# Kernel tuning notes

Hardware: AMD Instinct MI355X
Metric: run time of the kernel (lower is better)

## Reference

```python
import jax, jax.numpy as jnp
import numpy as np

D_MODEL = 1024
D_INTERNAL = 256


def setup_inputs() -> dict:
    key = jax.random.key(0)
    ks = jax.random.split(key, 12)
    s = 0.02
    return {
        "x": jax.random.normal(ks[0], (4, 2048, D_MODEL), dtype=jnp.float32),
        "Wq": jax.random.normal(ks[1], (D_MODEL, D_INTERNAL), dtype=jnp.float32) * s,
        "bq": jnp.zeros((D_INTERNAL,), dtype=jnp.float32),
        "Wk": jax.random.normal(ks[2], (D_MODEL, D_INTERNAL), dtype=jnp.float32) * s,
        "bk": jnp.zeros((D_INTERNAL,), dtype=jnp.float32),
        "Wv": jax.random.normal(ks[3], (D_MODEL, D_MODEL), dtype=jnp.float32) * s,
        "bv": jnp.zeros((D_MODEL,), dtype=jnp.float32),
        "W1": jax.random.normal(ks[4], (D_MODEL, D_MODEL), dtype=jnp.float32) * s,
        "b1": jnp.zeros((D_MODEL,), dtype=jnp.float32),
        "W2": jax.random.normal(ks[5], (D_MODEL, D_MODEL), dtype=jnp.float32) * s,
        "b2": jnp.zeros((D_MODEL,), dtype=jnp.float32),
    }


def reference(x, Wq, bq, Wk, bk, Wv, bv, W1, b1, W2, b2):
    # x: [B, S, D]
    S = x.shape[-2]
    q = x @ Wq + bq            # [B, S, Di]
    k = x @ Wk + bk            # [B, S, Di]
    v = x @ Wv + bv            # [B, S, D]
    scale = 1.0 / jnp.sqrt(jnp.asarray(q.shape[-1], dtype=x.dtype))
    scores = jnp.einsum('bqd,bkd->bqk', q, k) * scale  # [B, S, S]
    causal_mask = jnp.triu(jnp.ones((S, S), dtype=bool), k=1)
    scores = jnp.where(causal_mask, -jnp.inf, scores)
    attn = jax.nn.softmax(scores, axis=-1)             # [B, S, S]
    attention = jnp.einsum('bqk,bkd->bqd', attn, v)    # [B, S, D]
    h = x + attention
    ff = jax.nn.relu(h @ W1 + b1) @ W2 + b2
    return h + ff, attn
```

## Files before the change

kernel.cpp:

```cpp
#include <hip/hip_runtime.h>
#include <hip/hip_bf16.h>

#define BM 128
#define BN 128

typedef __bf16 bf16x8 __attribute__((ext_vector_type(8)));
typedef float f32x4 __attribute__((ext_vector_type(4)));
typedef unsigned short u16;

__device__ __forceinline__ u16 f2bf(float f) {
    __bf16 b = (__bf16)f;
    return __builtin_bit_cast(u16, b);
}
__device__ __forceinline__ float bf2f(u16 u) {
    __bf16 b = __builtin_bit_cast(__bf16, u);
    return (float)b;
}

__device__ __forceinline__ void gload_lds16(const void* g, void* l) {
    __builtin_amdgcn_global_load_lds(
        (const __attribute__((address_space(1))) void*)g,
        (__attribute__((address_space(3))) void*)l,
        16, 0, 0);
}

__device__ __forceinline__ bf16x8 lds_read_b128(const u16* p) {
    bf16x8 r;
    const __attribute__((address_space(3))) u16* lp =
        (const __attribute__((address_space(3))) u16*)p;
    asm volatile("ds_read_b128 %0, %1" : "=v"(r) : "v"(lp));
    return r;
}

template <int MODE>
__global__ __launch_bounds__(256)
void gemm_bt(const u16* __restrict__ A, int lda, long long a_bs,
             const u16* __restrict__ Bt, int ldb, long long b_bs,
             int Kdim, int ldc, long long c_bs,
             const float* __restrict__ bias, float scale,
             const void* __restrict__ resid, long long r_bs,
             void* __restrict__ out, int causal)
{
    int bx = blockIdx.x, by = blockIdx.y, bz = blockIdx.z;
    if (causal == 3) {
        const int t = blockIdx.x;
        int byy = (int)((sqrtf(8.f * (float)t + 1.f) - 1.f) * 0.5f);
        while ((byy + 1) * (byy + 2) / 2 <= t) byy++;
        while (byy * (byy + 1) / 2 > t) byy--;
        by = byy; bx = t - byy * (byy + 1) / 2; bz = blockIdx.y;
    }
    if (causal == 2 && bz >= 2) by = (int)gridDim.y - 1 - by;
    const int kend = (causal == 2) ? min(Kdim, (by + 1) * BM) : Kdim;

    A  += (long long)bz * a_bs;
    Bt += (long long)bz * b_bs;

    const int m0 = by * BM, n0 = bx * BN;
    const int tid = threadIdx.x;
    const int wave = tid >> 6, lane = tid & 63;
    const int wy = wave >> 1, wx = wave & 1;
    const int lr = lane >> 2, lc8 = (lane & 3) * 8;
    const int lane15 = lane & 15, kq = lane >> 4;

    __shared__ __align__(16) u16 As[2][BM * 32];
    __shared__ __align__(16) u16 Bs[2][BN * 32];

    f32x4 acc[4][4] = {};

    for (int k0 = 0; k0 < kend; k0 += 64) {
        __syncthreads();
        #pragma unroll
        for (int h = 0; h < 2; h++) {
            const int kh = k0 + h * 32 + lc8;
            #pragma unroll
            for (int it = 0; it < 2; it++) {
                const int row = wave * 16 + it * 64 + lr;
                gload_lds16(A  + (size_t)(m0 + row) * lda + kh,
                            &As[h][(wave * 16 + it * 64) * 32]);
                gload_lds16(Bt + (size_t)(n0 + row) * ldb + kh,
                            &Bs[h][(wave * 16 + it * 64) * 32]);
            }
        }
        __syncthreads();

        #pragma unroll
        for (int h = 0; h < 2; h++) {
            bf16x8 av[4], bv[4];
            #pragma unroll
            for (int i = 0; i < 4; i++)
                av[i] = *(const bf16x8*)&As[h][(wy * 64 + i * 16 + lane15) * 32 + kq * 8];
            #pragma unroll
            for (int j = 0; j < 4; j++)
                bv[j] = *(const bf16x8*)&Bs[h][(wx * 64 + j * 16 + lane15) * 32 + kq * 8];
            #pragma unroll
            for (int i = 0; i < 4; i++)
                #pragma unroll
                for (int j = 0; j < 4; j++)
                    acc[i][j] = __builtin_amdgcn_mfma_f32_16x16x32_bf16(av[i], bv[j], acc[i][j], 0, 0, 0);
        }
    }

    #pragma unroll
    for (int i = 0; i < 4; i++) {
        const int rl = m0 + wy * 64 + i * 16 + kq * 4;
        #pragma unroll
        for (int j = 0; j < 4; j++) {
            const int c = n0 + wx * 64 + j * 16 + lane15;
            #pragma unroll
            for (int rg = 0; rg < 4; rg++) {
                const int r = rl + rg;
                const size_t idx = (size_t)bz * c_bs + (size_t)r * ldc + c;
                const float v = acc[i][j][rg];
                if (MODE == 2) {
                    float p = __expf(v * scale);
                    if (c > r) p = 0.f;
                    ((u16*)out)[idx] = f2bf(p);
                } else if (MODE == 3) {
                    const u16* xr = (const u16*)resid;
                    const float linv = bias[(size_t)bz * 2048 + r];
                    const float h = bf2f(xr[(size_t)bz * r_bs + (size_t)r * ldc + c]) + v * linv;
                    ((u16*)out)[idx] = f2bf(h);
                }
            }
        }
    }
}

template <int MODE>
__global__ __launch_bounds__(512, 2)
void gemm_bt2(const u16* __restrict__ A, int lda,
              const u16* __restrict__ Bt, int ldb,
              int ldc,
              const float* __restrict__ bias,
              const void* __restrict__ resid,
              void* __restrict__ out)
{
    constexpr int NT = 16;
    const int gx = gridDim.x;
    const int nwg = gx * (int)gridDim.y;
    int lin = blockIdx.y * gx + blockIdx.x;
    lin = (lin & 7) * (nwg >> 3) + (lin >> 3);
    const int m0 = (lin / gx) * 256, n0 = (lin % gx) * 128;

    const int tid = threadIdx.x;
    const int wave = tid >> 6, lane = tid & 63;
    const int wr = wave >> 1, wc = wave & 1;
    const int lane15 = lane & 15, kq = lane >> 4;
    const int lr = lane >> 2;
    const int swzc8 = ((lane & 3) ^ ((lane >> 3) & 3)) * 8;
    const int lslot = lane15 * 32 + ((kq ^ ((lane15 >> 1) & 3)) * 8);

    __shared__ __align__(16) u16 As0[2][256 * 32];
    __shared__ __align__(16) u16 As1[2][256 * 32];
    __shared__ __align__(16) u16 As2[2][256 * 32];
    __shared__ __align__(16) u16 Bs0[2][128 * 32];
    __shared__ __align__(16) u16 Bs1[2][128 * 32];
    __shared__ __align__(16) u16 Bs2[2][128 * 32];

    f32x4 acc[4][4] = {};

    auto stage = [&](u16 (*Ad)[256 * 32], u16 (*Bd)[128 * 32], int tt) {
        #pragma unroll
        for (int h = 0; h < 2; h++) {
            const int kh = (tt << 6) + h * 32 + swzc8;
            #pragma unroll
            for (int it = 0; it < 2; it++) {
                const int row = wave * 16 + it * 128 + lr;
                gload_lds16(A + (size_t)(m0 + row) * lda + kh,
                            &Ad[h][(wave * 16 + it * 128) * 32]);
            }
            gload_lds16(Bt + (size_t)(n0 + wave * 16 + lr) * ldb + kh,
                        &Bd[h][(wave * 16) * 32]);
        }
    };

    stage(As0, Bs0, 0);
    stage(As1, Bs1, 1);

    #pragma unroll
    for (int t = 0; t < NT; t++) {
        u16 (*pAc)[256 * 32] = (t % 3 == 0) ? As0 : (t % 3 == 1) ? As1 : As2;
        u16 (*pBc)[128 * 32] = (t % 3 == 0) ? Bs0 : (t % 3 == 1) ? Bs1 : Bs2;
        if (t < NT - 1) asm volatile("s_waitcnt vmcnt(6)" ::: "memory");
        else            asm volatile("s_waitcnt vmcnt(0)" ::: "memory");
        __builtin_amdgcn_s_barrier();
        if (t + 2 < NT) {
            const int tn = (t + 2) % 3;
            u16 (*pAn)[256 * 32] = (tn == 0) ? As0 : (tn == 1) ? As1 : As2;
            u16 (*pBn)[128 * 32] = (tn == 0) ? Bs0 : (tn == 1) ? Bs1 : Bs2;
            stage(pAn, pBn, t + 2);
        }

        bf16x8 av0[4], bv0[4], av1[4], bv1[4];
        #pragma unroll
        for (int i = 0; i < 4; i++)
            av0[i] = lds_read_b128(&pAc[0][(wr * 4 + i) * 512 + lslot]);
        #pragma unroll
        for (int j = 0; j < 4; j++)
            bv0[j] = lds_read_b128(&pBc[0][(wc * 4 + j) * 512 + lslot]);
        #pragma unroll
        for (int i = 0; i < 4; i++)
            av1[i] = lds_read_b128(&pAc[1][(wr * 4 + i) * 512 + lslot]);
        #pragma unroll
        for (int j = 0; j < 4; j++)
            bv1[j] = lds_read_b128(&pBc[1][(wc * 4 + j) * 512 + lslot]);

        asm volatile("s_waitcnt lgkmcnt(8)" ::: "memory");
        __builtin_amdgcn_sched_barrier(0);
        __builtin_amdgcn_s_setprio(1);
        #pragma unroll
        for (int i = 0; i < 4; i++)
            #pragma unroll
            for (int j = 0; j < 4; j++)
                acc[i][j] = __builtin_amdgcn_mfma_f32_16x16x32_bf16(av0[i], bv0[j], acc[i][j], 0, 0, 0);
        __builtin_amdgcn_s_setprio(0);

        asm volatile("s_waitcnt lgkmcnt(0)" ::: "memory");
        __builtin_amdgcn_sched_barrier(0);
        __builtin_amdgcn_s_setprio(1);
        #pragma unroll
        for (int i = 0; i < 4; i++)
            #pragma unroll
            for (int j = 0; j < 4; j++)
                acc[i][j] = __builtin_amdgcn_mfma_f32_16x16x32_bf16(av1[i], bv1[j], acc[i][j], 0, 0, 0);
        __builtin_amdgcn_s_setprio(0);
    }

    if (MODE == 6 && n0 >= 512) {
        u16* o = (u16*)resid;
        #pragma unroll
        for (int i = 0; i < 4; i++) {
            const int r = m0 + wr * 64 + i * 16 + kq * 4;
            const size_t base = (size_t)(r >> 11) * 1024 * 2048 + (r & 2047);
            #pragma unroll
            for (int j = 0; j < 4; j++) {
                const int c = n0 + wc * 64 + j * 16 + lane15;
                const float bj = bias[c];
                ushort4 pk;
                pk.x = f2bf(acc[i][j][0] + bj);
                pk.y = f2bf(acc[i][j][1] + bj);
                pk.z = f2bf(acc[i][j][2] + bj);
                pk.w = f2bf(acc[i][j][3] + bj);
                *(ushort4*)&o[base + (size_t)(c - 512) * 2048] = pk;
            }
        }
    } else {
        #pragma unroll
        for (int i = 0; i < 4; i++) {
            const int rl = m0 + wr * 64 + i * 16 + kq * 4;
            #pragma unroll
            for (int j = 0; j < 4; j++) {
                const int c = n0 + wc * 64 + j * 16 + lane15;
                const float bj = bias[c];
                #pragma unroll
                for (int rg = 0; rg < 4; rg++) {
                    const int r = rl + rg;
                    const size_t idx = (size_t)r * ldc + c;
                    const float v = acc[i][j][rg];
                    if (MODE == 4) {
                        ((u16*)out)[idx] = f2bf(fmaxf(v + bj, 0.f));
                    } else if (MODE == 5) {
                        const u16* hb = (const u16*)resid;
                        ((float*)out)[idx] = v + bj + bf2f(hb[idx]);
                    } else if (MODE == 6) {
                        ((u16*)out)[idx] = f2bf(v + bj);
                    }
                }
            }
        }
    }
}

__global__ __launch_bounds__(256)
void prep_x(const float* __restrict__ x, u16* __restrict__ xb)
{
    const int N4 = 8388608 / 4;
    for (int i = blockIdx.x * blockDim.x + threadIdx.x; i < N4; i += gridDim.x * blockDim.x) {
        const float4 v = ((const float4*)x)[i];
        ushort4 o;
        o.x = f2bf(v.x); o.y = f2bf(v.y); o.z = f2bf(v.z); o.w = f2bf(v.w);
        ((ushort4*)xb)[i] = o;
    }
}

__global__ __launch_bounds__(256)
void prep_w(const float* __restrict__ Wq, const float* __restrict__ bq,
            const float* __restrict__ Wk, const float* __restrict__ bk,
            const float* __restrict__ Wv, const float* __restrict__ bv,
            const float* __restrict__ b1, const float* __restrict__ b2,
            const float* __restrict__ W1, const float* __restrict__ W2,
            u16* __restrict__ WqkT, u16* __restrict__ WvT,
            u16* __restrict__ W1T, u16* __restrict__ W2T, float* __restrict__ biasv)
{
    const int bid = blockIdx.x, tid = threadIdx.x;
    if (bid == 896) {
        for (int t = tid; t < 3584; t += 256) {
            if (t < 512)       biasv[t] = (t < 256) ? bq[t] : bk[t - 256];
            else if (t < 1536) biasv[t] = bv[t - 512];
            else if (t < 2560) biasv[t] = b1[t - 1536];
            else               biasv[t] = b2[t - 2560];
        }
        return;
    }
    const float* src; u16* dst; int ld_src, kt, nt, nbase;
    if (bid < 128) {
        const int job = bid >> 6, t = bid & 63;
        src = job ? Wk : Wq; ld_src = 256;
        kt = t >> 2; nt = t & 3; nbase = job * 256 + nt * 64;
        dst = WqkT;
    } else {
        const int j = bid - 128, w = j >> 8, t = j & 255;
        src = (w == 0) ? Wv : (w == 1) ? W1 : W2; ld_src = 1024;
        kt = t >> 4; nt = t & 15; nbase = nt * 64;
        dst = (w == 0) ? WvT : (w == 1) ? W1T : W2T;
    }
    const int k0 = kt * 64;
    const int n0s = (ld_src == 256) ? (nbase & 255) : nbase;

    __shared__ float tile[64][65];
    const int ri = tid >> 4, j4 = (tid & 15) * 4;
    #pragma unroll
    for (int rr = 0; rr < 4; rr++) {
        const int i = ri + rr * 16;
        const float4 v = *(const float4*)&src[(size_t)(k0 + i) * ld_src + n0s + j4];
        tile[j4 + 0][i] = v.x;
        tile[j4 + 1][i] = v.y;
        tile[j4 + 2][i] = v.z;
        tile[j4 + 3][i] = v.w;
    }
    __syncthreads();
    const int n = tid >> 2, ks = (tid & 3) * 16;
    ushort4 o[4];
    #pragma unroll
    for (int c = 0; c < 4; c++) {
        o[c].x = f2bf(tile[n][ks + c * 4 + 0]);
        o[c].y = f2bf(tile[n][ks + c * 4 + 1]);
        o[c].z = f2bf(tile[n][ks + c * 4 + 2]);
        o[c].w = f2bf(tile[n][ks + c * 4 + 3]);
    }
    u16* drow = &dst[(size_t)(nbase + n) * 1024 + k0 + ks];
    #pragma unroll
    for (int c = 0; c < 4; c++) *(ushort4*)&drow[c * 4] = o[c];
}

__device__ __forceinline__ float wave_sum(float v) {
    #pragma unroll
    for (int off = 32; off > 0; off >>= 1) v += __shfl_xor(v, off, 64);
    return v;
}

__global__ __launch_bounds__(256)
void norm_kernel(const u16* __restrict__ attnb, float* __restrict__ attn,
                 float* __restrict__ linv)
{
    const int S = 2048;
    const int row = blockIdx.x;
    const int q = row & (S - 1);
    const int kpad = (q + 128) & ~127;
    const u16* brow = attnb + (size_t)row * S;
    float* srow = attn + (size_t)row * S;
    __shared__ float red[4];
    const int tid = threadIdx.x, wv = tid >> 6, ln = tid & 63;
    const int k = tid * 8;

    float vals[8];
    float lsum = 0.f;
    if (k < kpad) {
        const ushort4 a = *(const ushort4*)&brow[k];
        const ushort4 b = *(const ushort4*)&brow[k + 4];
        vals[0] = bf2f(a.x); vals[1] = bf2f(a.y); vals[2] = bf2f(a.z); vals[3] = bf2f(a.w);
        vals[4] = bf2f(b.x); vals[5] = bf2f(b.y); vals[6] = bf2f(b.z); vals[7] = bf2f(b.w);
        #pragma unroll
        for (int c = 0; c < 8; c++) lsum += vals[c];
    }
    lsum = wave_sum(lsum);
    if (ln == 0) red[wv] = lsum;
    __syncthreads();
    const float rinv = 1.f / (red[0] + red[1] + red[2] + red[3]);

    float4 o0 = {0.f, 0.f, 0.f, 0.f}, o1 = {0.f, 0.f, 0.f, 0.f};
    if (k < kpad) {
        o0 = make_float4(vals[0] * rinv, vals[1] * rinv, vals[2] * rinv, vals[3] * rinv);
        o1 = make_float4(vals[4] * rinv, vals[5] * rinv, vals[6] * rinv, vals[7] * rinv);
    }
    *(float4*)&srow[k] = o0;
    *(float4*)&srow[k + 4] = o1;
    if (tid == 0) linv[row] = rinv;
}

extern "C" void kernel_launch(void* const* d_in, const int* in_sizes, int n_in,
                              void* d_out, int out_size, void* d_ws, size_t ws_size,
                              hipStream_t stream)
{
    const float* x  = (const float*)d_in[0];
    const float* Wq = (const float*)d_in[1];
    const float* bq = (const float*)d_in[2];
    const float* Wk = (const float*)d_in[3];
    const float* bk = (const float*)d_in[4];
    const float* Wv = (const float*)d_in[5];
    const float* bv = (const float*)d_in[6];
    const float* W1 = (const float*)d_in[7];
    const float* b1 = (const float*)d_in[8];
    const float* W2 = (const float*)d_in[9];
    const float* b2 = (const float*)d_in[10];

    const int B = 4, S = 2048, D = 1024, BS = B * S;

    char* ws = (char*)d_ws;
    u16*   xb    = (u16*)(ws + 0);
    u16*   WqkT  = (u16*)(ws + 16777216);
    u16*   WvT   = (u16*)(ws + 17825792);
    u16*   W1T   = (u16*)(ws + 19922944);
    u16*   W2T   = (u16*)(ws + 22020096);
    float* biasv = (float*)(ws + 24117248);
    u16*   QK    = (u16*)(ws + 24133632);
    u16*   Vt    = (u16*)(ws + 32522240);
    u16*   attnb = (u16*)(ws + 49299456);
    float* linv  = (float*)(ws + 83886080);
    u16*   hb    = xb;
    u16*   ff1   = attnb;

    float* out0 = (float*)d_out;
    float* attn = out0 + (size_t)BS * D;

    const dim3 blk(256);

    prep_x<<<dim3(1024), blk, 0, stream>>>(x, xb);
    prep_w<<<dim3(897), blk, 0, stream>>>(Wq, bq, Wk, bk, Wv, bv, b1, b2, W1, W2,
                                          WqkT, WvT, W1T, W2T, biasv);

    gemm_bt2<6><<<dim3(12, 32), dim3(512), 0, stream>>>(
        xb, 1024, WqkT, 1024, 512, biasv, Vt, QK);

    gemm_bt<2><<<dim3(136, 4, 1), blk, 0, stream>>>(
        QK, 512, (long long)S * 512, QK + 256, 512, (long long)S * 512,
        256, S, (long long)S * S, nullptr, 0.0625f, nullptr, 0, attnb, 3);

    norm_kernel<<<dim3(BS), blk, 0, stream>>>(attnb, attn, linv);

    gemm_bt<3><<<dim3(8, 16, 4), blk, 0, stream>>>(
        attnb, S, (long long)S * S, Vt, S, (long long)D * S,
        S, D, (long long)S * D, linv, 1.f, xb, (long long)S * D, hb, 2);

    gemm_bt2<4><<<dim3(8, 32), dim3(512), 0, stream>>>(
        hb, 1024, W1T, 1024, 1024, biasv + 1536, nullptr, ff1);

    gemm_bt2<5><<<dim3(8, 32), dim3(512), 0, stream>>>(
        ff1, 1024, W2T, 1024, 1024, biasv + 2560, hb, out0);
}
```

Before: 303.6 us.

## Unify GEMMs into 128x128 double-buffered kernel, reuse for causal attn@V

Replaces the 256x128 triple-buffered 512-thread GEMM with a generic 128x128 tile, 256-thread, double-buffered kernel that supports batching and a causal K limit. This kernel now serves the QKV projection, the causal attn@V product and both FFN layers. The aim is to give attn@V the faster swizzled direct-to-LDS pipeline and to raise occupancy and wave counts on the large GEMMs. In exchange the FFN and QKV GEMMs get smaller tiles with less reuse and a shallower prefetch pipeline.

```diff
diff --git a/kernel.cpp b/kernel.cpp
--- a/kernel.cpp
+++ b/kernel.cpp
@@ -49,8 +49,7 @@
         while (byy * (byy + 1) / 2 > t) byy--;
         by = byy; bx = t - byy * (byy + 1) / 2; bz = blockIdx.y;
     }
-    if (causal == 2 && bz >= 2) by = (int)gridDim.y - 1 - by;
-    const int kend = (causal == 2) ? min(Kdim, (by + 1) * BM) : Kdim;
+    const int kend = Kdim;
 
     A  += (long long)bz * a_bs;
     Bt += (long long)bz * b_bs;
@@ -115,11 +114,6 @@
                     float p = __expf(v * scale);
                     if (c > r) p = 0.f;
                     ((u16*)out)[idx] = f2bf(p);
-                } else if (MODE == 3) {
-                    const u16* xr = (const u16*)resid;
-                    const float linv = bias[(size_t)bz * 2048 + r];
-                    const float h = bf2f(xr[(size_t)bz * r_bs + (size_t)r * ldc + c]) + v * linv;
-                    ((u16*)out)[idx] = f2bf(h);
                 }
             }
         }
@@ -127,83 +121,86 @@
 }
 
 template <int MODE>
-__global__ __launch_bounds__(512, 2)
-void gemm_bt2(const u16* __restrict__ A, int lda,
-              const u16* __restrict__ Bt, int ldb,
-              int ldc,
+__global__ __launch_bounds__(256, 2)
+void gemm_bt3(const u16* __restrict__ A, int lda, long long a_bs,
+              const u16* __restrict__ Bt, int ldb, long long b_bs,
+              int Kdim, int ldc, long long c_bs,
               const float* __restrict__ bias,
-              const void* __restrict__ resid,
-              void* __restrict__ out)
-{
-    constexpr int NT = 16;
-    const int gx = gridDim.x;
-    const int nwg = gx * (int)gridDim.y;
-    int lin = blockIdx.y * gx + blockIdx.x;
-    lin = (lin & 7) * (nwg >> 3) + (lin >> 3);
-    const int m0 = (lin / gx) * 256, n0 = (lin % gx) * 128;
-
+              const void* __restrict__ resid, long long r_bs,
+              void* __restrict__ out, int causal)
+{
+    int bx = blockIdx.x, by = blockIdx.y;
+    const int bz = blockIdx.z;
+    if (causal == 0) {
+        const int gx = gridDim.x;
+        const int nwg = gx * (int)gridDim.y;
+        int lin = by * gx + bx;
+        lin = (lin & 7) * (nwg >> 3) + (lin >> 3);
+        by = lin / gx; bx = lin % gx;
+    } else if (causal == 2 && bz >= 2) {
+        by = (int)gridDim.y - 1 - by;
+    }
+    const int kend = (causal == 2) ? min(Kdim, (by + 1) * 128) : Kdim;
+    const int NT = kend >> 6;
+
+    A  += (long long)bz * a_bs;
+    Bt += (long long)bz * b_bs;
+
+    const int m0 = by * 128, n0 = bx * 128;
     const int tid = threadIdx.x;
     const int wave = tid >> 6, lane = tid & 63;
-    const int wr = wave >> 1, wc = wave & 1;
+    const int wy = wave >> 1, wx = wave & 1;
     const int lane15 = lane & 15, kq = lane >> 4;
     const int lr = lane >> 2;
     const int swzc8 = ((lane & 3) ^ ((lane >> 3) & 3)) * 8;
     const int lslot = lane15 * 32 + ((kq ^ ((lane15 >> 1) & 3)) * 8);
 
-    __shared__ __align__(16) u16 As0[2][256 * 32];
-    __shared__ __align__(16) u16 As1[2][256 * 32];
-    __shared__ __align__(16) u16 As2[2][256 * 32];
-    __shared__ __align__(16) u16 Bs0[2][128 * 32];
-    __shared__ __align__(16) u16 Bs1[2][128 * 32];
-    __shared__ __align__(16) u16 Bs2[2][128 * 32];
+    __shared__ __align__(16) u16 As[2][2][128 * 32];
+    __shared__ __align__(16) u16 Bs[2][2][128 * 32];
 
     f32x4 acc[4][4] = {};
 
-    auto stage = [&](u16 (*Ad)[256 * 32], u16 (*Bd)[128 * 32], int tt) {
+    auto stage = [&](int buf, int tt) {
         #pragma unroll
         for (int h = 0; h < 2; h++) {
             const int kh = (tt << 6) + h * 32 + swzc8;
             #pragma unroll
             for (int it = 0; it < 2; it++) {
-                const int row = wave * 16 + it * 128 + lr;
+                const int row = wave * 16 + it * 64 + lr;
                 gload_lds16(A + (size_t)(m0 + row) * lda + kh,
-                            &Ad[h][(wave * 16 + it * 128) * 32]);
+                            &As[buf][h][(wave * 16 + it * 64) * 32]);
+                gload_lds16(Bt + (size_t)(n0 + row) * ldb + kh,
+                            &Bs[buf][h][(wave * 16 + it * 64) * 32]);
             }
-            gload_lds16(Bt + (size_t)(n0 + wave * 16 + lr) * ldb + kh,
-                        &Bd[h][(wave * 16) * 32]);
         }
     };
 
-    stage(As0, Bs0, 0);
-    stage(As1, Bs1, 1);
-
-    #pragma unroll
+    stage(0, 0);
+
     for (int t = 0; t < NT; t++) {
-        u16 (*pAc)[256 * 32] = (t % 3 == 0) ? As0 : (t % 3 == 1) ? As1 : As2;
-        u16 (*pBc)[128 * 32] = (t % 3 == 0) ? Bs0 : (t % 3 == 1) ? Bs1 : Bs2;
-        if (t < NT - 1) asm volatile("s_waitcnt vmcnt(6)" ::: "memory");
-        else            asm volatile("s_waitcnt vmcnt(0)" ::: "memory");
+        const int cur = t & 1;
+        if (t) __builtin_amdgcn_s_barrier();
+        if (t + 1 < NT) {
+            stage(cur ^ 1, t + 1);
+            asm volatile("s_waitcnt vmcnt(8)" ::: "memory");
+        } else {
+            asm volatile("s_waitcnt vmcnt(0)" ::: "memory");
+        }
         __builtin_amdgcn_s_barrier();
-        if (t + 2 < NT) {
-            const int tn = (t + 2) % 3;
-            u16 (*pAn)[256 * 32] = (tn == 0) ? As0 : (tn == 1) ? As1 : As2;
-            u16 (*pBn)[128 * 32] = (tn == 0) ? Bs0 : (tn == 1) ? Bs1 : Bs2;
-            stage(pAn, pBn, t + 2);
-        }
 
         bf16x8 av0[4], bv0[4], av1[4], bv1[4];
         #pragma unroll
         for (int i = 0; i < 4; i++)
-            av0[i] = lds_read_b128(&pAc[0][(wr * 4 + i) * 512 + lslot]);
+            av0[i] = lds_read_b128(&As[cur][0][(wy * 64 + i * 16) * 32 + lslot]);
         #pragma unroll
         for (int j = 0; j < 4; j++)
-            bv0[j] = lds_read_b128(&pBc[0][(wc * 4 + j) * 512 + lslot]);
+            bv0[j] = lds_read_b128(&Bs[cur][0][(wx * 64 + j * 16) * 32 + lslot]);
         #pragma unroll
         for (int i = 0; i < 4; i++)
-            av1[i] = lds_read_b128(&pAc[1][(wr * 4 + i) * 512 + lslot]);
+            av1[i] = lds_read_b128(&As[cur][1][(wy * 64 + i * 16) * 32 + lslot]);
         #pragma unroll
         for (int j = 0; j < 4; j++)
-            bv1[j] = lds_read_b128(&pBc[1][(wc * 4 + j) * 512 + lslot]);
+            bv1[j] = lds_read_b128(&Bs[cur][1][(wx * 64 + j * 16) * 32 + lslot]);
 
         asm volatile("s_waitcnt lgkmcnt(8)" ::: "memory");
         __builtin_amdgcn_sched_barrier(0);
@@ -230,11 +227,11 @@
         u16* o = (u16*)resid;
         #pragma unroll
         for (int i = 0; i < 4; i++) {
-            const int r = m0 + wr * 64 + i * 16 + kq * 4;
+            const int r = m0 + wy * 64 + i * 16 + kq * 4;
             const size_t base = (size_t)(r >> 11) * 1024 * 2048 + (r & 2047);
             #pragma unroll
             for (int j = 0; j < 4; j++) {
-                const int c = n0 + wc * 64 + j * 16 + lane15;
+                const int c = n0 + wx * 64 + j * 16 + lane15;
                 const float bj = bias[c];
                 ushort4 pk;
                 pk.x = f2bf(acc[i][j][0] + bj);
@@ -247,21 +244,27 @@
     } else {
         #pragma unroll
         for (int i = 0; i < 4; i++) {
-            const int rl = m0 + wr * 64 + i * 16 + kq * 4;
+            const int rl = m0 + wy * 64 + i * 16 + kq * 4;
             #pragma unroll
             for (int j = 0; j < 4; j++) {
-                const int c = n0 + wc * 64 + j * 16 + lane15;
-                const float bj = bias[c];
+                const int c = n0 + wx * 64 + j * 16 + lane15;
+                float bj = 0.f;
+                if (MODE == 4 || MODE == 5 || MODE == 6) bj = bias[c];
                 #pragma unroll
                 for (int rg = 0; rg < 4; rg++) {
                     const int r = rl + rg;
-                    const size_t idx = (size_t)r * ldc + c;
+                    const size_t idx = (size_t)bz * c_bs + (size_t)r * ldc + c;
                     const float v = acc[i][j][rg];
-                    if (MODE == 4) {
+                    if (MODE == 3) {
+                        const u16* xr = (const u16*)resid;
+                        const float linv = bias[(size_t)bz * 2048 + r];
+                        const float h = bf2f(xr[(size_t)bz * r_bs + (size_t)r * ldc + c]) + v * linv;
+                        ((u16*)out)[idx] = f2bf(h);
+                    } else if (MODE == 4) {
                         ((u16*)out)[idx] = f2bf(fmaxf(v + bj, 0.f));
                     } else if (MODE == 5) {
                         const u16* hb = (const u16*)resid;
-                        ((float*)out)[idx] = v + bj + bf2f(hb[idx]);
+                        ((float*)out)[idx] = v + bj + bf2f(hb[(size_t)r * ldc + c]);
                     } else if (MODE == 6) {
                         ((u16*)out)[idx] = f2bf(v + bj);
                     }
@@ -429,8 +432,9 @@
     prep_w<<<dim3(897), blk, 0, stream>>>(Wq, bq, Wk, bk, Wv, bv, b1, b2, W1, W2,
                                           WqkT, WvT, W1T, W2T, biasv);
 
-    gemm_bt2<6><<<dim3(12, 32), dim3(512), 0, stream>>>(
-        xb, 1024, WqkT, 1024, 512, biasv, Vt, QK);
+    gemm_bt3<6><<<dim3(12, 64, 1), blk, 0, stream>>>(
+        xb, 1024, 0, WqkT, 1024, 0, 1024, 512, 0,
+        biasv, Vt, 0, QK, 0);
 
     gemm_bt<2><<<dim3(136, 4, 1), blk, 0, stream>>>(
         QK, 512, (long long)S * 512, QK + 256, 512, (long long)S * 512,
@@ -438,13 +442,15 @@
 
     norm_kernel<<<dim3(BS), blk, 0, stream>>>(attnb, attn, linv);
 
-    gemm_bt<3><<<dim3(8, 16, 4), blk, 0, stream>>>(
+    gemm_bt3<3><<<dim3(8, 16, 4), blk, 0, stream>>>(
         attnb, S, (long long)S * S, Vt, S, (long long)D * S,
-        S, D, (long long)S * D, linv, 1.f, xb, (long long)S * D, hb, 2);
-
-    gemm_bt2<4><<<dim3(8, 32), dim3(512), 0, stream>>>(
-        hb, 1024, W1T, 1024, 1024, biasv + 1536, nullptr, ff1);
-
-    gemm_bt2<5><<<dim3(8, 32), dim3(512), 0, stream>>>(
-        ff1, 1024, W2T, 1024, 1024, biasv + 2560, hb, out0);
-}
+        S, D, (long long)S * D, linv, xb, (long long)S * D, hb, 2);
+
+    gemm_bt3<4><<<dim3(8, 64, 1), blk, 0, stream>>>(
+        hb, 1024, 0, W1T, 1024, 0, 1024, 1024, 0,
+        biasv + 1536, nullptr, 0, ff1, 0);
+
+    gemm_bt3<5><<<dim3(8, 64, 1), blk, 0, stream>>>(
+        ff1, 1024, 0, W2T, 1024, 0, 1024, 1024, 0,
+        biasv + 2560, hb, 0, out0, 0);
+}
```

Measured after the change: 292.1 us. 1.04x faster.
